# Optimization experiments

Hardware: AMD Instinct MI355X
Metric: run time of the kernel (lower is better)

## Reference

```python
import jax, jax.numpy as jnp
import numpy as np

KD = KH = KW = 3  # kernel_size
OR = OC = OZ = 22  # valid-conv output dims for 24^3 input, stride 1


def _extract_patches(x):
    # x: (B, D, H, W, C) -> patches: (B, P, KD*KH*KW*C), P = OR*OC*OZ
    slabs = []
    for di in range(KD):
        for dj in range(KH):
            for dk in range(KW):
                slabs.append(x[:, di:di + OR, dj:dj + OC, dk:dk + OZ, :])
    # (KD*KH*KW, B, OR, OC, OZ, C) -> (B, OR, OC, OZ, KD*KH*KW, C)
    p = jnp.stack(slabs, axis=0)
    p = jnp.moveaxis(p, 0, 4)
    B = x.shape[0]
    C = x.shape[-1]
    return p.reshape(B, OR * OC * OZ, KD * KH * KW * C)


def setup_inputs() -> dict:
    key = jax.random.key(0)
    k1, k2 = jax.random.split(key)
    B, D, C, F = 2, 24, 8, 8
    P = OR * OC * OZ            # 10648 spatial locations
    K = KD * KH * KW * C        # 216 patch features
    x = jax.random.normal(k1, (B, D, D, D, C), dtype=jnp.float32)
    kernel = jax.random.normal(k2, (P, K, F), dtype=jnp.float32) * 0.05
    bias = jnp.zeros((OR, OC, OZ, F), dtype=jnp.float32)
    return {"x": x, "kernel": kernel, "bias": bias}


def reference(x, kernel, bias):
    # Locally-connected 3D conv (unshared weights), channels_last, valid padding,
    # stride 1, linear activation (activation=None in the Keras layer).
    B = x.shape[0]
    F = kernel.shape[-1]
    patches = _extract_patches(x)                    # (B, P, K)
    out = jnp.einsum('bpk,pkf->bpf', patches, kernel)  # per-location matmul
    out = out.reshape(B, OR, OC, OZ, F) + bias[None]
    return out
```

## Files before the change

kernel.cpp:

```cpp
#include <hip/hip_runtime.h>


constexpr int P_TOT = 22 * 22 * 22;
constexpr int KTOT  = 216;
constexpr int XB    = 24 * 24 * 24 * 8;
constexpr int NV4   = KTOT * 8 / 4;

__global__ __launch_bounds__(256) void lc3d_kernel(
    const float* __restrict__ x,
    const float* __restrict__ kern,
    const float* __restrict__ bias,
    float* __restrict__ out)
{
    __shared__ float xl[4][2 * KTOT];

    const int tid  = threadIdx.x;
    const int wave = tid >> 6;
    const int lane = tid & 63;
    const int p    = blockIdx.x * 4 + wave;

    const int oz  = p % 22;
    const int t   = p / 22;
    const int oc  = t % 22;
    const int orr = t / 22;
    const int xbase = orr * 4608 + oc * 192 + oz * 8;

    float* xw = xl[wave];

    #pragma unroll
    for (int r = 0; r < 2; ++r) {
        const int t4 = lane + r * 64;
        if (t4 < 108) {
            const int seg = t4 / 6;
            const int wi  = t4 - seg * 6;
            const int b   = seg / 9;
            const int s   = seg - b * 9;
            const int di  = s / 3;
            const int dj  = s - di * 3;
            const float4 v = *reinterpret_cast<const float4*>(
                x + (size_t)b * XB + xbase + di * 4608 + dj * 192 + wi * 4);
            *reinterpret_cast<float4*>(xw + seg * 24 + wi * 4) = v;
        }
    }

    const float4* kp4 = reinterpret_cast<const float4*>(kern) + (size_t)p * NV4;
    const int k0 = lane >> 1;

    float4 a0 = make_float4(0.f, 0.f, 0.f, 0.f);
    float4 a1 = make_float4(0.f, 0.f, 0.f, 0.f);

    auto body = [&](int j, int k) {
        const float4 kv = kp4[j];
        const float x0 = xw[k];
        const float x1 = xw[KTOT + k];
        a0.x = fmaf(x0, kv.x, a0.x);
        a0.y = fmaf(x0, kv.y, a0.y);
        a0.z = fmaf(x0, kv.z, a0.z);
        a0.w = fmaf(x0, kv.w, a0.w);
        a1.x = fmaf(x1, kv.x, a1.x);
        a1.y = fmaf(x1, kv.y, a1.y);
        a1.z = fmaf(x1, kv.z, a1.z);
        a1.w = fmaf(x1, kv.w, a1.w);
    };

    #pragma unroll
    for (int i = 0; i < 6; ++i) body(lane + 64 * i, k0 + 32 * i);
    if (lane < 48) body(lane + 384, k0 + 192);

    #pragma unroll
    for (int m = 2; m <= 32; m <<= 1) {
        a0.x += __shfl_xor(a0.x, m, 64);
        a0.y += __shfl_xor(a0.y, m, 64);
        a0.z += __shfl_xor(a0.z, m, 64);
        a0.w += __shfl_xor(a0.w, m, 64);
        a1.x += __shfl_xor(a1.x, m, 64);
        a1.y += __shfl_xor(a1.y, m, 64);
        a1.z += __shfl_xor(a1.z, m, 64);
        a1.w += __shfl_xor(a1.w, m, 64);
    }

    if (lane < 2) {
        const int fb = lane * 4;
        const float4 bv = *reinterpret_cast<const float4*>(bias + (size_t)p * 8 + fb);
        float4 o0, o1;
        o0.x = a0.x + bv.x;  o0.y = a0.y + bv.y;  o0.z = a0.z + bv.z;  o0.w = a0.w + bv.w;
        o1.x = a1.x + bv.x;  o1.y = a1.y + bv.y;  o1.z = a1.z + bv.z;  o1.w = a1.w + bv.w;
        *reinterpret_cast<float4*>(out + (size_t)p * 8 + fb) = o0;
        *reinterpret_cast<float4*>(out + (size_t)P_TOT * 8 + (size_t)p * 8 + fb) = o1;
    }
}

extern "C" void kernel_launch(void* const* d_in, const int* in_sizes, int n_in,
                              void* d_out, int out_size, void* d_ws, size_t ws_size,
                              hipStream_t stream) {
    const float* x    = (const float*)d_in[0];
    const float* kern = (const float*)d_in[1];
    const float* bias = (const float*)d_in[2];
    float* out        = (float*)d_out;

    lc3d_kernel<<<P_TOT / 4, 256, 0, stream>>>(x, kern, bias, out);
}
```

Baseline: 18.86 us.

## Process four locations per wave with register double-buffered prefetch

Each wave now handles four consecutive output locations instead of one. The weights and input patch for the next location are loaded into registers while the FMAs for the current one run, and LDS is double-buffered per wave. The goal is to hide global-load latency on the kernel stream, which dominates this memory-bound kernel. The cost is more registers and four times fewer blocks, which lowers occupancy and parallelism. The LDS write for the next location happens without any barrier, which is safe only because each wave uses its own buffers.

```diff
diff --git a/kernel.cpp b/kernel.cpp
--- a/kernel.cpp
+++ b/kernel.cpp
@@ -4,7 +4,10 @@
 constexpr int P_TOT = 22 * 22 * 22;
 constexpr int KTOT  = 216;
 constexpr int XB    = 24 * 24 * 24 * 8;
-constexpr int NV4   = KTOT * 8 / 4;
+constexpr int NV4   = 432;
+constexpr int PPW   = 4;
+constexpr int PPB   = 16;
+constexpr int NBLK  = (P_TOT + PPB - 1) / PPB;
 
 __global__ __launch_bounds__(256) void lc3d_kernel(
     const float* __restrict__ x,
@@ -12,81 +15,107 @@
     const float* __restrict__ bias,
     float* __restrict__ out)
 {
-    __shared__ float xl[4][2 * KTOT];
+    __shared__ float xl[4][2][2 * KTOT];
 
     const int tid  = threadIdx.x;
     const int wave = tid >> 6;
     const int lane = tid & 63;
-    const int p    = blockIdx.x * 4 + wave;
+    const int p0   = blockIdx.x * PPB + wave * PPW;
 
-    const int oz  = p % 22;
-    const int t   = p / 22;
-    const int oc  = t % 22;
-    const int orr = t / 22;
-    const int xbase = orr * 4608 + oc * 192 + oz * 8;
+    float* xw0 = xl[wave][0];
+    float* xw1 = xl[wave][1];
 
-    float* xw = xl[wave];
+    const int t4b  = lane + 64;
+    const bool mB  = (t4b < 108);
+    const int segA = lane / 6,      wiA = lane - segA * 6;
+    const int bA   = segA / 9,      sA  = segA - bA * 9;
+    const int diA  = sA / 3,        djA = sA - diA * 3;
+    const int xoffA = bA * XB + diA * 4608 + djA * 192 + wiA * 4;
+    const int loffA = segA * 24 + wiA * 4;
+    const int segB = t4b / 6,       wiB = t4b - segB * 6;
+    const int bB   = segB / 9,      sB  = segB - bB * 9;
+    const int diB  = sB / 3,        djB = sB - diB * 3;
+    const int xoffB = bB * XB + diB * 4608 + djB * 192 + wiB * 4;
+    const int loffB = segB * 24 + wiB * 4;
+
+    const int k0 = lane >> 1;
+
+    float4 bw[2][7];
+    float4 bxA[2], bxB[2];
+
+    auto xbase_of = [](int p) {
+        const int oz = p % 22, t = p / 22, oc = t % 22, orr = t / 22;
+        return orr * 4608 + oc * 192 + oz * 8;
+    };
+    auto loadX = [&](int p, float4& a, float4& b) {
+        const int xb = xbase_of(p);
+        a = *reinterpret_cast<const float4*>(x + xb + xoffA);
+        if (mB) b = *reinterpret_cast<const float4*>(x + xb + xoffB);
+    };
+    auto loadW = [&](int p, float4* dst) {
+        const float4* kp = reinterpret_cast<const float4*>(kern) + (size_t)p * NV4;
+        #pragma unroll
+        for (int i = 0; i < 6; ++i) dst[i] = kp[lane + 64 * i];
+        if (lane < 48) dst[6] = kp[lane + 384];
+    };
+    auto writeX = [&](float* xw, const float4& a, const float4& b) {
+        *reinterpret_cast<float4*>(xw + loffA) = a;
+        if (mB) *reinterpret_cast<float4*>(xw + loffB) = b;
+    };
+
+    if (p0 < P_TOT) {
+        loadX(p0, bxA[0], bxB[0]);
+        loadW(p0, bw[0]);
+        writeX(xw0, bxA[0], bxB[0]);
+    }
 
     #pragma unroll
-    for (int r = 0; r < 2; ++r) {
-        const int t4 = lane + r * 64;
-        if (t4 < 108) {
-            const int seg = t4 / 6;
-            const int wi  = t4 - seg * 6;
-            const int b   = seg / 9;
-            const int s   = seg - b * 9;
-            const int di  = s / 3;
-            const int dj  = s - di * 3;
-            const float4 v = *reinterpret_cast<const float4*>(
-                x + (size_t)b * XB + xbase + di * 4608 + dj * 192 + wi * 4);
-            *reinterpret_cast<float4*>(xw + seg * 24 + wi * 4) = v;
+    for (int i = 0; i < PPW; ++i) {
+        const int p = p0 + i;
+        if (p >= P_TOT) break;
+        const int cur = i & 1;
+        float* xwc = (cur == 0) ? xw0 : xw1;
+        float* xwn = (cur == 0) ? xw1 : xw0;
+        const bool pf = (i + 1 < PPW) && (p + 1 < P_TOT);
+
+        if (pf) {
+            loadX(p + 1, bxA[cur ^ 1], bxB[cur ^ 1]);
+            loadW(p + 1, bw[cur ^ 1]);
         }
-    }
 
-    const float4* kp4 = reinterpret_cast<const float4*>(kern) + (size_t)p * NV4;
-    const int k0 = lane >> 1;
+        float4 a0 = make_float4(0.f, 0.f, 0.f, 0.f);
+        float4 a1 = make_float4(0.f, 0.f, 0.f, 0.f);
+        auto fma8 = [&](const float4& kv, int k) {
+            const float x0 = xwc[k];
+            const float x1 = xwc[KTOT + k];
+            a0.x = fmaf(x0, kv.x, a0.x);  a0.y = fmaf(x0, kv.y, a0.y);
+            a0.z = fmaf(x0, kv.z, a0.z);  a0.w = fmaf(x0, kv.w, a0.w);
+            a1.x = fmaf(x1, kv.x, a1.x);  a1.y = fmaf(x1, kv.y, a1.y);
+            a1.z = fmaf(x1, kv.z, a1.z);  a1.w = fmaf(x1, kv.w, a1.w);
+        };
+        #pragma unroll
+        for (int c = 0; c < 6; ++c) fma8(bw[cur][c], k0 + 32 * c);
+        if (lane < 48) fma8(bw[cur][6], k0 + 192);
 
-    float4 a0 = make_float4(0.f, 0.f, 0.f, 0.f);
-    float4 a1 = make_float4(0.f, 0.f, 0.f, 0.f);
+        if (pf) writeX(xwn, bxA[cur ^ 1], bxB[cur ^ 1]);
 
-    auto body = [&](int j, int k) {
-        const float4 kv = kp4[j];
-        const float x0 = xw[k];
-        const float x1 = xw[KTOT + k];
-        a0.x = fmaf(x0, kv.x, a0.x);
-        a0.y = fmaf(x0, kv.y, a0.y);
-        a0.z = fmaf(x0, kv.z, a0.z);
-        a0.w = fmaf(x0, kv.w, a0.w);
-        a1.x = fmaf(x1, kv.x, a1.x);
-        a1.y = fmaf(x1, kv.y, a1.y);
-        a1.z = fmaf(x1, kv.z, a1.z);
-        a1.w = fmaf(x1, kv.w, a1.w);
-    };
+        #pragma unroll
+        for (int m = 2; m <= 32; m <<= 1) {
+            a0.x += __shfl_xor(a0.x, m, 64);  a0.y += __shfl_xor(a0.y, m, 64);
+            a0.z += __shfl_xor(a0.z, m, 64);  a0.w += __shfl_xor(a0.w, m, 64);
+            a1.x += __shfl_xor(a1.x, m, 64);  a1.y += __shfl_xor(a1.y, m, 64);
+            a1.z += __shfl_xor(a1.z, m, 64);  a1.w += __shfl_xor(a1.w, m, 64);
+        }
 
-    #pragma unroll
-    for (int i = 0; i < 6; ++i) body(lane + 64 * i, k0 + 32 * i);
-    if (lane < 48) body(lane + 384, k0 + 192);
-
-    #pragma unroll
-    for (int m = 2; m <= 32; m <<= 1) {
-        a0.x += __shfl_xor(a0.x, m, 64);
-        a0.y += __shfl_xor(a0.y, m, 64);
-        a0.z += __shfl_xor(a0.z, m, 64);
-        a0.w += __shfl_xor(a0.w, m, 64);
-        a1.x += __shfl_xor(a1.x, m, 64);
-        a1.y += __shfl_xor(a1.y, m, 64);
-        a1.z += __shfl_xor(a1.z, m, 64);
-        a1.w += __shfl_xor(a1.w, m, 64);
-    }
-
-    if (lane < 2) {
-        const int fb = lane * 4;
-        const float4 bv = *reinterpret_cast<const float4*>(bias + (size_t)p * 8 + fb);
-        float4 o0, o1;
-        o0.x = a0.x + bv.x;  o0.y = a0.y + bv.y;  o0.z = a0.z + bv.z;  o0.w = a0.w + bv.w;
-        o1.x = a1.x + bv.x;  o1.y = a1.y + bv.y;  o1.z = a1.z + bv.z;  o1.w = a1.w + bv.w;
-        *reinterpret_cast<float4*>(out + (size_t)p * 8 + fb) = o0;
-        *reinterpret_cast<float4*>(out + (size_t)P_TOT * 8 + (size_t)p * 8 + fb) = o1;
+        if (lane < 2) {
+            const int fb = lane * 4;
+            const float4 bv = *reinterpret_cast<const float4*>(bias + (size_t)p * 8 + fb);
+            float4 o0, o1;
+            o0.x = a0.x + bv.x;  o0.y = a0.y + bv.y;  o0.z = a0.z + bv.z;  o0.w = a0.w + bv.w;
+            o1.x = a1.x + bv.x;  o1.y = a1.y + bv.y;  o1.z = a1.z + bv.z;  o1.w = a1.w + bv.w;
+            *reinterpret_cast<float4*>(out + (size_t)p * 8 + fb) = o0;
+            *reinterpret_cast<float4*>(out + (size_t)P_TOT * 8 + (size_t)p * 8 + fb) = o1;
+        }
     }
 }
 
@@ -98,5 +127,5 @@
     const float* bias = (const float*)d_in[2];
     float* out        = (float*)d_out;
 
-    lc3d_kernel<<<P_TOT / 4, 256, 0, stream>>>(x, kern, bias, out);
+    lc3d_kernel<<<NBLK, 256, 0, stream>>>(x, kern, bias, out);
 }
```

Result: slower. 21.74 us (+15.3%).
